# Kernel optimization log

Measured on AMD Instinct MI355X. Metric: run time of the kernel, lower is better.

Reference implementation:

```python
import jax, jax.numpy as jnp
import numpy as np

N = 8192
D_IN = 128
D_OUT = 128
EPS = 1e-06


def setup_inputs() -> dict:
    key = jax.random.key(0)
    k1, k2, k3, k4 = jax.random.split(key, 4)
    x = jax.random.normal(k1, (N, D_IN), dtype=jnp.float32)
    adj = jax.random.uniform(k2, (N, N), dtype=jnp.float32)
    # nn.Linear(in_features, out_features) params, PyTorch default-ish init scale
    bound = 1.0 / np.sqrt(D_IN)
    W = jax.random.uniform(k3, (D_OUT, D_IN), dtype=jnp.float32, minval=-bound, maxval=bound)
    b = jax.random.uniform(k4, (D_OUT,), dtype=jnp.float32, minval=-bound, maxval=bound)
    return {"x": x, "adj": adj, "W": W, "b": b}


def reference(x, adj, W, b):
    # D^{-1/2} A D^{-1/2}: the diag-matmul chain is mathematically a
    # row/col broadcast scale of adj, so express it that way (same math).
    d_inv_sqrt = 1.0 / jnp.sqrt(adj.sum(axis=1) + EPS)  # [N]
    adj_norm = d_inv_sqrt[:, None] * adj * d_inv_sqrt[None, :]  # [N, N]
    h = adj_norm @ x  # [N, D_IN]
    return h @ W.T + b  # [N, D_OUT]
```

## Files before the change

### kernel.cpp

```cpp
#include <hip/hip_runtime.h>
#include <hip/hip_bf16.h>

#define NN 8192
#define DIN 128
#define DOUT 128

typedef __bf16 bf16;
typedef __bf16 bf16x4 __attribute__((ext_vector_type(4)));
typedef __bf16 bf16x8 __attribute__((ext_vector_type(8)));
typedef float f32x4 __attribute__((ext_vector_type(4)));

__global__ __launch_bounds__(256) void k1_rowsum(const float* __restrict__ adj,
                                                 float* __restrict__ dinv) {
    int wave = threadIdx.x >> 6;
    int lane = threadIdx.x & 63;
    int row  = blockIdx.x * 4 + wave;
    const float4* p = reinterpret_cast<const float4*>(adj + (size_t)row * NN);
    float s = 0.f;
    #pragma unroll
    for (int i = 0; i < 32; ++i) {
        float4 v = p[lane + i * 64];
        s += (v.x + v.y) + (v.z + v.w);
    }
    #pragma unroll
    for (int off = 32; off > 0; off >>= 1) s += __shfl_down(s, off, 64);
    if (lane == 0) dinv[row] = rsqrtf(s + 1e-6f);
}

__global__ __launch_bounds__(256) void k2_transpose(const float* __restrict__ x,
                                                    const float* __restrict__ dinv,
                                                    bf16* __restrict__ yT) {
    __shared__ bf16 T[DIN][136];
    __shared__ float dl[128];
    int t  = threadIdx.x;
    int j0 = blockIdx.x * 128;
    if (t < 128) dl[t] = dinv[j0 + t];
    __syncthreads();
    #pragma unroll
    for (int s = 0; s < 16; ++s) {
        int i  = t + s * 256;
        int j  = i >> 5;
        int c4 = i & 31;
        float4 v = *reinterpret_cast<const float4*>(x + (size_t)(j0 + j) * DIN + c4 * 4);
        float d = dl[j];
        T[c4 * 4 + 0][j] = (bf16)(v.x * d);
        T[c4 * 4 + 1][j] = (bf16)(v.y * d);
        T[c4 * 4 + 2][j] = (bf16)(v.z * d);
        T[c4 * 4 + 3][j] = (bf16)(v.w * d);
    }
    __syncthreads();
    #pragma unroll
    for (int s = 0; s < 8; ++s) {
        int i  = t + s * 256;
        int c  = i >> 4;
        int j8 = i & 15;
        *reinterpret_cast<uint4*>(yT + (size_t)c * NN + j0 + j8 * 8) =
            *reinterpret_cast<const uint4*>(&T[c][j8 * 8]);
    }
}

#define LDA 72
#define LDB 72

__global__ __launch_bounds__(256) void k3_gemm(const float* __restrict__ adj,
                                               const bf16* __restrict__ yT,
                                               float* __restrict__ hp) {
    __shared__ bf16 Asm[32 * LDA];
    __shared__ bf16 Bsm[128 * LDB];
    int t     = threadIdx.x;
    int mb    = blockIdx.x >> 1;
    int split = blockIdx.x & 1;
    int m0    = mb * 32;
    int k0    = split * 4096;
    int lane  = t & 63;
    int wn    = t >> 6;
    int mrow  = lane & 15;
    int quad  = lane >> 4;

    f32x4 acc[2][2] = {};

    const float* aptr = adj + (size_t)m0 * NN + k0;
    const bf16*  bptr = yT + k0;

    for (int kk = 0; kk < 64; ++kk) {
        int col0 = kk * 64;
        __syncthreads();
        #pragma unroll
        for (int s = 0; s < 2; ++s) {
            int i   = t + s * 256;
            int row = i >> 4;
            int c4  = i & 15;
            float4 v = *reinterpret_cast<const float4*>(aptr + (size_t)row * NN + col0 + c4 * 4);
            bf16x4 bv = { (bf16)v.x, (bf16)v.y, (bf16)v.z, (bf16)v.w };
            *reinterpret_cast<bf16x4*>(&Asm[row * LDA + c4 * 4]) = bv;
        }
        #pragma unroll
        for (int s = 0; s < 4; ++s) {
            int i  = t + s * 256;
            int n  = i >> 3;
            int c8 = i & 7;
            uint4 v = *reinterpret_cast<const uint4*>(bptr + (size_t)n * NN + col0 + c8 * 8);
            *reinterpret_cast<uint4*>(&Bsm[n * LDB + c8 * 8]) = v;
        }
        __syncthreads();
        #pragma unroll
        for (int ks = 0; ks < 2; ++ks) {
            bf16x8 af[2], bfr[2];
            #pragma unroll
            for (int mi = 0; mi < 2; ++mi)
                af[mi] = *reinterpret_cast<const bf16x8*>(
                    &Asm[(mi * 16 + mrow) * LDA + ks * 32 + quad * 8]);
            #pragma unroll
            for (int ni = 0; ni < 2; ++ni)
                bfr[ni] = *reinterpret_cast<const bf16x8*>(
                    &Bsm[(wn * 32 + ni * 16 + mrow) * LDB + ks * 32 + quad * 8]);
            #pragma unroll
            for (int mi = 0; mi < 2; ++mi)
                #pragma unroll
                for (int ni = 0; ni < 2; ++ni)
                    acc[mi][ni] = __builtin_amdgcn_mfma_f32_16x16x32_bf16(
                        af[mi], bfr[ni], acc[mi][ni], 0, 0, 0);
        }
    }
    float* out = hp + (size_t)split * (NN * DIN);
    #pragma unroll
    for (int mi = 0; mi < 2; ++mi)
        #pragma unroll
        for (int ni = 0; ni < 2; ++ni) {
            int col = wn * 32 + ni * 16 + mrow;
            #pragma unroll
            for (int r = 0; r < 4; ++r) {
                int row = m0 + mi * 16 + quad * 4 + r;
                out[(size_t)row * DIN + col] = acc[mi][ni][r];
            }
        }
}

__global__ __launch_bounds__(256) void k4_out(const float* __restrict__ hp,
                                              const float* __restrict__ dinv,
                                              const float* __restrict__ W,
                                              const float* __restrict__ bias,
                                              float* __restrict__ out) {
    __shared__ float Wl[128 * 132];
    __shared__ float hl[32 * 132];
    __shared__ float bl[128];
    int t  = threadIdx.x;
    int i0 = blockIdx.x * 32;
    if (t < 128) bl[t] = bias[t];
    #pragma unroll
    for (int s = 0; s < 16; ++s) {
        int i  = t + s * 256;
        int o  = i >> 5;
        int c4 = i & 31;
        *reinterpret_cast<float4*>(&Wl[o * 132 + c4 * 4]) =
            *reinterpret_cast<const float4*>(W + o * 128 + c4 * 4);
    }
    const float* hp0 = hp;
    const float* hp1 = hp + (size_t)NN * DIN;
    #pragma unroll
    for (int s = 0; s < 4; ++s) {
        int i   = t + s * 256;
        int row = i >> 5;
        int c4  = i & 31;
        size_t g = (size_t)(i0 + row) * DIN + c4 * 4;
        float4 v0 = *reinterpret_cast<const float4*>(hp0 + g);
        float4 v1 = *reinterpret_cast<const float4*>(hp1 + g);
        float d = dinv[i0 + row];
        float4 hv = { (v0.x + v1.x) * d, (v0.y + v1.y) * d,
                      (v0.z + v1.z) * d, (v0.w + v1.w) * d };
        *reinterpret_cast<float4*>(&hl[row * 132 + c4 * 4]) = hv;
    }
    __syncthreads();
    int o = t & 127;
    int g = t >> 7;
    float acc[16];
    #pragma unroll
    for (int r = 0; r < 16; ++r) acc[r] = bl[o];
    for (int c4 = 0; c4 < 32; ++c4) {
        float4 w4 = *reinterpret_cast<const float4*>(&Wl[o * 132 + c4 * 4]);
        #pragma unroll
        for (int r = 0; r < 16; ++r) {
            float4 h4 = *reinterpret_cast<const float4*>(&hl[(g * 16 + r) * 132 + c4 * 4]);
            acc[r] += h4.x * w4.x + h4.y * w4.y + h4.z * w4.z + h4.w * w4.w;
        }
    }
    #pragma unroll
    for (int r = 0; r < 16; ++r)
        out[(size_t)(i0 + g * 16 + r) * DOUT + o] = acc[r];
}

extern "C" void kernel_launch(void* const* d_in, const int* in_sizes, int n_in,
                              void* d_out, int out_size, void* d_ws, size_t ws_size,
                              hipStream_t stream) {
    const float* x   = (const float*)d_in[0];
    const float* adj = (const float*)d_in[1];
    const float* W   = (const float*)d_in[2];
    const float* b   = (const float*)d_in[3];
    float* out = (float*)d_out;
    char* ws = (char*)d_ws;
    float* dinv = (float*)ws;
    bf16*  yT   = (bf16*)(ws + (1 << 20));
    float* hp   = (float*)(ws + (3 << 20));

    k1_rowsum  <<<NN / 4, 256, 0, stream>>>(adj, dinv);
    k2_transpose<<<NN / 128, 256, 0, stream>>>(x, dinv, yT);
    k3_gemm    <<<(NN / 32) * 2, 256, 0, stream>>>(adj, yT, hp);
    k4_out     <<<NN / 32, 256, 0, stream>>>(hp, dinv, W, b, out);
}
```

Measured before the change: 506.1 us.

## Convert adj to bf16 during rowsum, prefetch GEMM tiles, split-K into four

The rowsum kernel now also writes a bf16 copy of adj, so the GEMM streams half the bytes per tile and skips per-tile conversion. The GEMM loop preloads the next tile into registers while the current one sits in shared memory, and split-K grows from 2 to 4 so more blocks run. The cost is an extra 128MB write plus a 128MB read of the bf16 matrix, on top of the fp32 read that was already needed. More split-K partial sums also have to be reduced in the output kernel.

```diff
diff --git a/kernel.cpp b/kernel.cpp
--- a/kernel.cpp
+++ b/kernel.cpp
@@ -10,21 +10,27 @@
 typedef __bf16 bf16x8 __attribute__((ext_vector_type(8)));
 typedef float f32x4 __attribute__((ext_vector_type(4)));
 
-__global__ __launch_bounds__(256) void k1_rowsum(const float* __restrict__ adj,
-                                                 float* __restrict__ dinv) {
-    int wave = threadIdx.x >> 6;
-    int lane = threadIdx.x & 63;
-    int row  = blockIdx.x * 4 + wave;
+__global__ __launch_bounds__(256) void k1_rowsum_cvt(const float* __restrict__ adj,
+                                                     float* __restrict__ dinv,
+                                                     bf16* __restrict__ adjb) {
+    int row = blockIdx.x;
+    int t   = threadIdx.x;
     const float4* p = reinterpret_cast<const float4*>(adj + (size_t)row * NN);
+    bf16x4* q = reinterpret_cast<bf16x4*>(adjb + (size_t)row * NN);
     float s = 0.f;
     #pragma unroll
-    for (int i = 0; i < 32; ++i) {
-        float4 v = p[lane + i * 64];
+    for (int i = 0; i < 8; ++i) {
+        float4 v = p[t + i * 256];
+        bf16x4 b = { (bf16)v.x, (bf16)v.y, (bf16)v.z, (bf16)v.w };
+        q[t + i * 256] = b;
         s += (v.x + v.y) + (v.z + v.w);
     }
     #pragma unroll
     for (int off = 32; off > 0; off >>= 1) s += __shfl_down(s, off, 64);
-    if (lane == 0) dinv[row] = rsqrtf(s + 1e-6f);
+    __shared__ float r4[4];
+    if ((t & 63) == 0) r4[t >> 6] = s;
+    __syncthreads();
+    if (t == 0) dinv[row] = rsqrtf(((r4[0] + r4[1]) + (r4[2] + r4[3])) + 1e-6f);
 }
 
 __global__ __launch_bounds__(256) void k2_transpose(const float* __restrict__ x,
@@ -62,45 +68,47 @@
 #define LDA 72
 #define LDB 72
 
-__global__ __launch_bounds__(256) void k3_gemm(const float* __restrict__ adj,
+__global__ __launch_bounds__(256) void k3_gemm(const bf16* __restrict__ adjb,
                                                const bf16* __restrict__ yT,
                                                float* __restrict__ hp) {
     __shared__ bf16 Asm[32 * LDA];
     __shared__ bf16 Bsm[128 * LDB];
     int t     = threadIdx.x;
-    int mb    = blockIdx.x >> 1;
-    int split = blockIdx.x & 1;
+    int mb    = blockIdx.x >> 2;
+    int split = blockIdx.x & 3;
     int m0    = mb * 32;
-    int k0    = split * 4096;
+    int k0    = split * 2048;
     int lane  = t & 63;
     int wn    = t >> 6;
     int mrow  = lane & 15;
     int quad  = lane >> 4;
 
+    int arow = t >> 3;
+    int ac8  = t & 7;
+
     f32x4 acc[2][2] = {};
 
-    const float* aptr = adj + (size_t)m0 * NN + k0;
-    const bf16*  bptr = yT + k0;
-
-    for (int kk = 0; kk < 64; ++kk) {
-        int col0 = kk * 64;
+    const bf16* ap = adjb + (size_t)(m0 + arow) * NN + k0 + ac8 * 8;
+    const bf16* bp = yT + (size_t)arow * NN + k0 + ac8 * 8;
+
+    uint4 av = *reinterpret_cast<const uint4*>(ap);
+    uint4 bv[4];
+    #pragma unroll
+    for (int s = 0; s < 4; ++s)
+        bv[s] = *reinterpret_cast<const uint4*>(bp + (size_t)(s * 32) * NN);
+
+    for (int kk = 0; kk < 32; ++kk) {
         __syncthreads();
-        #pragma unroll
-        for (int s = 0; s < 2; ++s) {
-            int i   = t + s * 256;
-            int row = i >> 4;
-            int c4  = i & 15;
-            float4 v = *reinterpret_cast<const float4*>(aptr + (size_t)row * NN + col0 + c4 * 4);
-            bf16x4 bv = { (bf16)v.x, (bf16)v.y, (bf16)v.z, (bf16)v.w };
-            *reinterpret_cast<bf16x4*>(&Asm[row * LDA + c4 * 4]) = bv;
-        }
-        #pragma unroll
-        for (int s = 0; s < 4; ++s) {
-            int i  = t + s * 256;
-            int n  = i >> 3;
-            int c8 = i & 7;
-            uint4 v = *reinterpret_cast<const uint4*>(bptr + (size_t)n * NN + col0 + c8 * 8);
-            *reinterpret_cast<uint4*>(&Bsm[n * LDB + c8 * 8]) = v;
+        *reinterpret_cast<uint4*>(&Asm[arow * LDA + ac8 * 8]) = av;
+        #pragma unroll
+        for (int s = 0; s < 4; ++s)
+            *reinterpret_cast<uint4*>(&Bsm[(arow + s * 32) * LDB + ac8 * 8]) = bv[s];
+        if (kk < 31) {
+            int col0 = (kk + 1) * 64;
+            av = *reinterpret_cast<const uint4*>(ap + col0);
+            #pragma unroll
+            for (int s = 0; s < 4; ++s)
+                bv[s] = *reinterpret_cast<const uint4*>(bp + (size_t)(s * 32) * NN + col0);
         }
         __syncthreads();
         #pragma unroll
@@ -155,19 +163,21 @@
         *reinterpret_cast<float4*>(&Wl[o * 132 + c4 * 4]) =
             *reinterpret_cast<const float4*>(W + o * 128 + c4 * 4);
     }
-    const float* hp0 = hp;
-    const float* hp1 = hp + (size_t)NN * DIN;
     #pragma unroll
     for (int s = 0; s < 4; ++s) {
         int i   = t + s * 256;
         int row = i >> 5;
         int c4  = i & 31;
         size_t g = (size_t)(i0 + row) * DIN + c4 * 4;
-        float4 v0 = *reinterpret_cast<const float4*>(hp0 + g);
-        float4 v1 = *reinterpret_cast<const float4*>(hp1 + g);
+        float4 a0 = *reinterpret_cast<const float4*>(hp + g);
+        float4 a1 = *reinterpret_cast<const float4*>(hp + (size_t)NN * DIN + g);
+        float4 a2 = *reinterpret_cast<const float4*>(hp + (size_t)2 * NN * DIN + g);
+        float4 a3 = *reinterpret_cast<const float4*>(hp + (size_t)3 * NN * DIN + g);
         float d = dinv[i0 + row];
-        float4 hv = { (v0.x + v1.x) * d, (v0.y + v1.y) * d,
-                      (v0.z + v1.z) * d, (v0.w + v1.w) * d };
+        float4 hv = { ((a0.x + a1.x) + (a2.x + a3.x)) * d,
+                      ((a0.y + a1.y) + (a2.y + a3.y)) * d,
+                      ((a0.z + a1.z) + (a2.z + a3.z)) * d,
+                      ((a0.w + a1.w) + (a2.w + a3.w)) * d };
         *reinterpret_cast<float4*>(&hl[row * 132 + c4 * 4]) = hv;
     }
     __syncthreads();
@@ -199,11 +209,12 @@
     float* out = (float*)d_out;
     char* ws = (char*)d_ws;
     float* dinv = (float*)ws;
-    bf16*  yT   = (bf16*)(ws + (1 << 20));
-    float* hp   = (float*)(ws + (3 << 20));
-
-    k1_rowsum  <<<NN / 4, 256, 0, stream>>>(adj, dinv);
-    k2_transpose<<<NN / 128, 256, 0, stream>>>(x, dinv, yT);
-    k3_gemm    <<<(NN / 32) * 2, 256, 0, stream>>>(adj, yT, hp);
-    k4_out     <<<NN / 32, 256, 0, stream>>>(hp, dinv, W, b, out);
-}
+    bf16*  yT   = (bf16*)(ws + (1u << 20));
+    float* hp   = (float*)(ws + (4u << 20));
+    bf16*  adjb = (bf16*)(ws + (32u << 20));
+
+    k1_rowsum_cvt<<<NN, 256, 0, stream>>>(adj, dinv, adjb);
+    k2_transpose <<<NN / 128, 256, 0, stream>>>(x, dinv, yT);
+    k3_gemm      <<<(NN / 32) * 4, 256, 0, stream>>>(adjb, yT, hp);
+    k4_out       <<<NN / 32, 256, 0, stream>>>(hp, dinv, W, b, out);
+}
```

Result: slower. 580.0 us (+14.6%).
